# Kernel optimization log

Measured on AMD Instinct MI355X. Metric: run time of the kernel, lower is better.

The kernel has to match this reference:

```python
import jax, jax.numpy as jnp
import numpy as np

B, S, V = 64, 2048, 256

def setup_inputs() -> dict:
    key = jax.random.key(0)
    k1, k2 = jax.random.split(key)
    logits = jax.random.normal(k1, (B, S, V), dtype=jnp.float32)
    prior_knowledge_matrix = jax.random.normal(k2, (V, V), dtype=jnp.float32)
    return {"logits": logits, "prior_knowledge_matrix": prior_knowledge_matrix}

def reference(logits, prior_knowledge_matrix):
    # log-softmax over tag dim
    d = jax.nn.log_softmax(logits, axis=-1)  # [B, S, V]
    # out[b, i] = d[b, i, :] @ M @ d[b, i+1, :]  for i in [0, S-2]
    # fused diagonal-only bilinear form over adjacent positions
    left = jnp.einsum('bsv,vw->bsw', d[:, :-1, :], prior_knowledge_matrix)  # [B, S-1, V]
    out = jnp.einsum('bsw,bsw->bs', left, d[:, 1:, :])  # [B, S-1]
    return out
```

## Files before the change

### kernel.cpp

```cpp
#include <hip/hip_runtime.h>
#include <hip/hip_bf16.h>


#define BQ   32
#define ROWS (BQ + 1)
#define LDA  264

typedef __attribute__((ext_vector_type(8))) short short8;
typedef __attribute__((ext_vector_type(4))) float f32x4;

__device__ __forceinline__ unsigned short f2bf(float f) {
    unsigned int u = __float_as_uint(f);
    unsigned int r = (u + 0x7fffu + ((u >> 16) & 1u)) >> 16;
    return (unsigned short)r;
}
__device__ __forceinline__ float bf2f(unsigned short u) {
    return __uint_as_float(((unsigned int)u) << 16);
}

__global__ void pk_prep(const float* __restrict__ M, unsigned short* __restrict__ mt) {
    int idx = blockIdx.x * 256 + threadIdx.x;
    int n = idx >> 8, k = idx & 255;
    mt[idx] = f2bf(M[k * 256 + n]);
}

__global__ __launch_bounds__(256, 6) void pk_main(const float* __restrict__ logits,
                                                  const unsigned short* __restrict__ mt,
                                                  float* __restrict__ out) {
    __shared__ unsigned short dA[ROWS * LDA];
    __shared__ float partial[BQ][4];

    const int tid  = threadIdx.x;
    const int lane = tid & 63;
    const int wid  = tid >> 6;
    const int b     = blockIdx.x >> 6;
    const int chunk = blockIdx.x & 63;
    const int i0    = chunk * BQ;
    const int nrows = min(ROWS, 2048 - i0);

    const int l15 = lane & 15;
    const int kg  = (lane >> 4) * 8;
    const unsigned short* mw = mt + ((size_t)(wid * 64 + l15)) * 256 + kg;

    {
        const int sub = lane >> 4;
        const float* rowbase = logits + ((size_t)(b * 2048 + i0)) * 256 + l15 * 4;
        const int r0 = wid * 4 + sub;
        const int r1 = 16 + wid * 4 + sub;
        const int r2b = 32 + wid * 4 + sub;
        const bool has2 = (r2b < nrows);

        float4 x0[4], x1[4], x2[4];
        #pragma unroll
        for (int p = 0; p < 4; ++p)
            x0[p] = *reinterpret_cast<const float4*>(rowbase + (size_t)r0 * 256 + p * 64);
        #pragma unroll
        for (int p = 0; p < 4; ++p)
            x1[p] = *reinterpret_cast<const float4*>(rowbase + (size_t)r1 * 256 + p * 64);
        if (has2) {
            #pragma unroll
            for (int p = 0; p < 4; ++p)
                x2[p] = *reinterpret_cast<const float4*>(rowbase + (size_t)r2b * 256 + p * 64);
        }

        {
            float s = 0.f;
            #pragma unroll
            for (int p = 0; p < 4; ++p)
                s += __expf(x0[p].x) + __expf(x0[p].y) + __expf(x0[p].z) + __expf(x0[p].w);
            #pragma unroll
            for (int off = 8; off; off >>= 1) s += __shfl_xor(s, off);
            float lse = __logf(s);
            #pragma unroll
            for (int p = 0; p < 4; ++p) {
                ushort4 pk;
                pk.x = f2bf(x0[p].x - lse); pk.y = f2bf(x0[p].y - lse);
                pk.z = f2bf(x0[p].z - lse); pk.w = f2bf(x0[p].w - lse);
                *reinterpret_cast<ushort4*>(&dA[r0 * LDA + l15 * 4 + p * 64]) = pk;
            }
        }
        {
            float s = 0.f;
            #pragma unroll
            for (int p = 0; p < 4; ++p)
                s += __expf(x1[p].x) + __expf(x1[p].y) + __expf(x1[p].z) + __expf(x1[p].w);
            #pragma unroll
            for (int off = 8; off; off >>= 1) s += __shfl_xor(s, off);
            float lse = __logf(s);
            #pragma unroll
            for (int p = 0; p < 4; ++p) {
                ushort4 pk;
                pk.x = f2bf(x1[p].x - lse); pk.y = f2bf(x1[p].y - lse);
                pk.z = f2bf(x1[p].z - lse); pk.w = f2bf(x1[p].w - lse);
                *reinterpret_cast<ushort4*>(&dA[r1 * LDA + l15 * 4 + p * 64]) = pk;
            }
        }
        if (has2) {
            float s = 0.f;
            #pragma unroll
            for (int p = 0; p < 4; ++p)
                s += __expf(x2[p].x) + __expf(x2[p].y) + __expf(x2[p].z) + __expf(x2[p].w);
            #pragma unroll
            for (int off = 8; off; off >>= 1) s += __shfl_xor(s, off);
            float lse = __logf(s);
            #pragma unroll
            for (int p = 0; p < 4; ++p) {
                ushort4 pk;
                pk.x = f2bf(x2[p].x - lse); pk.y = f2bf(x2[p].y - lse);
                pk.z = f2bf(x2[p].z - lse); pk.w = f2bf(x2[p].w - lse);
                *reinterpret_cast<ushort4*>(&dA[r2b * LDA + l15 * 4 + p * 64]) = pk;
            }
        }
    }

    f32x4 acc[2][4];
    #pragma unroll
    for (int a = 0; a < 2; ++a)
        #pragma unroll
        for (int n = 0; n < 4; ++n) acc[a][n] = (f32x4){0.f, 0.f, 0.f, 0.f};

    short8 bA[4], bB[4];
    #pragma unroll
    for (int n = 0; n < 4; ++n)
        bA[n] = *reinterpret_cast<const short8*>(mw + n * 16 * 256);

    __syncthreads();

    #pragma unroll
    for (int kt = 0; kt < 8; ++kt) {
        short8* cur = (kt & 1) ? bB : bA;
        short8* nxt = (kt & 1) ? bA : bB;
        if (kt < 7) {
            #pragma unroll
            for (int n = 0; n < 4; ++n)
                nxt[n] = *reinterpret_cast<const short8*>(mw + n * 16 * 256 + (kt + 1) * 32);
        }
        short8 aF[2];
        #pragma unroll
        for (int a = 0; a < 2; ++a)
            aF[a] = *reinterpret_cast<const short8*>(&dA[(a * 16 + l15) * LDA + kt * 32 + kg]);
        #pragma unroll
        for (int a = 0; a < 2; ++a)
            #pragma unroll
            for (int n = 0; n < 4; ++n)
                acc[a][n] = __builtin_amdgcn_mfma_f32_16x16x32_bf16(aF[a], cur[n], acc[a][n], 0, 0, 0);
    }

    const int rg = lane >> 4;
    #pragma unroll
    for (int a = 0; a < 2; ++a) {
        #pragma unroll
        for (int r2 = 0; r2 < 4; ++r2) {
            int row = a * 16 + rg * 4 + r2;
            float p = 0.f;
            #pragma unroll
            for (int n = 0; n < 4; ++n) {
                int col = wid * 64 + n * 16 + l15;
                p += acc[a][n][r2] * bf2f(dA[(row + 1) * LDA + col]);
            }
            #pragma unroll
            for (int off = 8; off; off >>= 1) p += __shfl_xor(p, off);
            if (l15 == 0) partial[row][wid] = p;
        }
    }
    __syncthreads();

    if (tid < BQ) {
        float4 pv = *reinterpret_cast<const float4*>(partial[tid]);
        int i = i0 + tid;
        if (i < 2047) out[(size_t)b * 2047 + i] = pv.x + pv.y + pv.z + pv.w;
    }
}

extern "C" void kernel_launch(void* const* d_in, const int* in_sizes, int n_in,
                              void* d_out, int out_size, void* d_ws, size_t ws_size,
                              hipStream_t stream) {
    const float* logits = (const float*)d_in[0];
    const float* M      = (const float*)d_in[1];
    float* out          = (float*)d_out;
    unsigned short* mt  = (unsigned short*)d_ws;

    pk_prep<<<256, 256, 0, stream>>>(M, mt);
    pk_main<<<64 * 64, 256, 0, stream>>>(logits, mt, out);
}
```

Measured before the change: 233.0 us.

## Double row tile to 64 with 8 waves, DPP row reductions, vectorized prep

Each block now handles 64 sequence rows with 512 threads (8 waves), each wave computing 32 output columns over 4 row tiles. The one-row halo reload per block shrinks from 1/32 to 1/64 of the rows, and block count halves. Shuffle-based 16-lane reductions are replaced with DPP row operations, and the matrix transpose/convert prep reads float4 with 64 blocks. The risk is lower occupancy from the larger LDS footprint and bigger blocks, plus fewer blocks for load balancing.

```diff
diff --git a/kernel.cpp b/kernel.cpp
--- a/kernel.cpp
+++ b/kernel.cpp
@@ -2,7 +2,7 @@
 #include <hip/hip_bf16.h>
 
 
-#define BQ   32
+#define BQ   64
 #define ROWS (BQ + 1)
 #define LDA  264
 
@@ -18,49 +18,65 @@
     return __uint_as_float(((unsigned int)u) << 16);
 }
 
+template<int CTRL>
+__device__ __forceinline__ float dpp_xadd(float x) {
+    int y = __builtin_amdgcn_update_dpp(0, __builtin_bit_cast(int, x), CTRL, 0xF, 0xF, true);
+    return x + __builtin_bit_cast(float, y);
+}
+__device__ __forceinline__ float row16_sum(float s) {
+    s = dpp_xadd<0xB1>(s);
+    s = dpp_xadd<0x4E>(s);
+    s = dpp_xadd<0x141>(s);
+    s = dpp_xadd<0x140>(s);
+    return s;
+}
+
 __global__ void pk_prep(const float* __restrict__ M, unsigned short* __restrict__ mt) {
     int idx = blockIdx.x * 256 + threadIdx.x;
-    int n = idx >> 8, k = idx & 255;
-    mt[idx] = f2bf(M[k * 256 + n]);
+    int k  = idx >> 6;
+    int n4 = (idx & 63) * 4;
+    float4 v = *reinterpret_cast<const float4*>(M + (size_t)k * 256 + n4);
+    mt[(n4 + 0) * 256 + k] = f2bf(v.x);
+    mt[(n4 + 1) * 256 + k] = f2bf(v.y);
+    mt[(n4 + 2) * 256 + k] = f2bf(v.z);
+    mt[(n4 + 3) * 256 + k] = f2bf(v.w);
 }
 
-__global__ __launch_bounds__(256, 6) void pk_main(const float* __restrict__ logits,
+__global__ __launch_bounds__(512, 6) void pk_main(const float* __restrict__ logits,
                                                   const unsigned short* __restrict__ mt,
                                                   float* __restrict__ out) {
     __shared__ unsigned short dA[ROWS * LDA];
-    __shared__ float partial[BQ][4];
+    __shared__ float partial[BQ][8];
 
     const int tid  = threadIdx.x;
     const int lane = tid & 63;
     const int wid  = tid >> 6;
-    const int b     = blockIdx.x >> 6;
-    const int chunk = blockIdx.x & 63;
+    const int b     = blockIdx.x >> 5;
+    const int chunk = blockIdx.x & 31;
     const int i0    = chunk * BQ;
     const int nrows = min(ROWS, 2048 - i0);
 
     const int l15 = lane & 15;
-    const int kg  = (lane >> 4) * 8;
-    const unsigned short* mw = mt + ((size_t)(wid * 64 + l15)) * 256 + kg;
+    const int rg  = lane >> 4;
+    const int kg  = rg * 8;
 
     {
-        const int sub = lane >> 4;
         const float* rowbase = logits + ((size_t)(b * 2048 + i0)) * 256 + l15 * 4;
-        const int r0 = wid * 4 + sub;
-        const int r1 = 16 + wid * 4 + sub;
-        const int r2b = 32 + wid * 4 + sub;
-        const bool has2 = (r2b < nrows);
+        const int r0 = wid * 4 + rg;
+        const int r1 = r0 + 32;
+        const bool hasB = (r0 == 0) && (nrows == ROWS);
 
-        float4 x0[4], x1[4], x2[4];
+        float4 x0[4], x1[4], xb[4];
         #pragma unroll
         for (int p = 0; p < 4; ++p)
             x0[p] = *reinterpret_cast<const float4*>(rowbase + (size_t)r0 * 256 + p * 64);
         #pragma unroll
         for (int p = 0; p < 4; ++p)
             x1[p] = *reinterpret_cast<const float4*>(rowbase + (size_t)r1 * 256 + p * 64);
-        if (has2) {
+        if (hasB) {
             #pragma unroll
             for (int p = 0; p < 4; ++p)
-                x2[p] = *reinterpret_cast<const float4*>(rowbase + (size_t)r2b * 256 + p * 64);
+                xb[p] = *reinterpret_cast<const float4*>(rowbase + (size_t)64 * 256 + p * 64);
         }
 
         {
@@ -68,9 +84,7 @@
             #pragma unroll
             for (int p = 0; p < 4; ++p)
                 s += __expf(x0[p].x) + __expf(x0[p].y) + __expf(x0[p].z) + __expf(x0[p].w);
-            #pragma unroll
-            for (int off = 8; off; off >>= 1) s += __shfl_xor(s, off);
-            float lse = __logf(s);
+            float lse = __logf(row16_sum(s));
             #pragma unroll
             for (int p = 0; p < 4; ++p) {
                 ushort4 pk;
@@ -84,9 +98,7 @@
             #pragma unroll
             for (int p = 0; p < 4; ++p)
                 s += __expf(x1[p].x) + __expf(x1[p].y) + __expf(x1[p].z) + __expf(x1[p].w);
-            #pragma unroll
-            for (int off = 8; off; off >>= 1) s += __shfl_xor(s, off);
-            float lse = __logf(s);
+            float lse = __logf(row16_sum(s));
             #pragma unroll
             for (int p = 0; p < 4; ++p) {
                 ushort4 pk;
@@ -95,33 +107,32 @@
                 *reinterpret_cast<ushort4*>(&dA[r1 * LDA + l15 * 4 + p * 64]) = pk;
             }
         }
-        if (has2) {
+        if (hasB) {
             float s = 0.f;
             #pragma unroll
             for (int p = 0; p < 4; ++p)
-                s += __expf(x2[p].x) + __expf(x2[p].y) + __expf(x2[p].z) + __expf(x2[p].w);
-            #pragma unroll
-            for (int off = 8; off; off >>= 1) s += __shfl_xor(s, off);
-            float lse = __logf(s);
+                s += __expf(xb[p].x) + __expf(xb[p].y) + __expf(xb[p].z) + __expf(xb[p].w);
+            float lse = __logf(row16_sum(s));
             #pragma unroll
             for (int p = 0; p < 4; ++p) {
                 ushort4 pk;
-                pk.x = f2bf(x2[p].x - lse); pk.y = f2bf(x2[p].y - lse);
-                pk.z = f2bf(x2[p].z - lse); pk.w = f2bf(x2[p].w - lse);
-                *reinterpret_cast<ushort4*>(&dA[r2b * LDA + l15 * 4 + p * 64]) = pk;
+                pk.x = f2bf(xb[p].x - lse); pk.y = f2bf(xb[p].y - lse);
+                pk.z = f2bf(xb[p].z - lse); pk.w = f2bf(xb[p].w - lse);
+                *reinterpret_cast<ushort4*>(&dA[64 * LDA + l15 * 4 + p * 64]) = pk;
             }
         }
     }
 
-    f32x4 acc[2][4];
+    f32x4 acc[4][2];
     #pragma unroll
-    for (int a = 0; a < 2; ++a)
+    for (int a = 0; a < 4; ++a)
         #pragma unroll
-        for (int n = 0; n < 4; ++n) acc[a][n] = (f32x4){0.f, 0.f, 0.f, 0.f};
+        for (int n = 0; n < 2; ++n) acc[a][n] = (f32x4){0.f, 0.f, 0.f, 0.f};
 
-    short8 bA[4], bB[4];
+    const unsigned short* mw = mt + ((size_t)(wid * 32 + l15)) * 256 + kg;
+    short8 bA[2], bB[2];
     #pragma unroll
-    for (int n = 0; n < 4; ++n)
+    for (int n = 0; n < 2; ++n)
         bA[n] = *reinterpret_cast<const short8*>(mw + n * 16 * 256);
 
     __syncthreads();
@@ -132,43 +143,44 @@
         short8* nxt = (kt & 1) ? bA : bB;
         if (kt < 7) {
             #pragma unroll
-            for (int n = 0; n < 4; ++n)
+            for (int n = 0; n < 2; ++n)
                 nxt[n] = *reinterpret_cast<const short8*>(mw + n * 16 * 256 + (kt + 1) * 32);
         }
-        short8 aF[2];
+        short8 aF[4];
         #pragma unroll
-        for (int a = 0; a < 2; ++a)
+        for (int a = 0; a < 4; ++a)
             aF[a] = *reinterpret_cast<const short8*>(&dA[(a * 16 + l15) * LDA + kt * 32 + kg]);
         #pragma unroll
-        for (int a = 0; a < 2; ++a)
+        for (int a = 0; a < 4; ++a)
             #pragma unroll
-            for (int n = 0; n < 4; ++n)
+            for (int n = 0; n < 2; ++n)
                 acc[a][n] = __builtin_amdgcn_mfma_f32_16x16x32_bf16(aF[a], cur[n], acc[a][n], 0, 0, 0);
     }
 
-    const int rg = lane >> 4;
     #pragma unroll
-    for (int a = 0; a < 2; ++a) {
+    for (int a = 0; a < 4; ++a) {
         #pragma unroll
         for (int r2 = 0; r2 < 4; ++r2) {
             int row = a * 16 + rg * 4 + r2;
             float p = 0.f;
             #pragma unroll
-            for (int n = 0; n < 4; ++n) {
-                int col = wid * 64 + n * 16 + l15;
+            for (int n = 0; n < 2; ++n) {
+                int col = wid * 32 + n * 16 + l15;
                 p += acc[a][n][r2] * bf2f(dA[(row + 1) * LDA + col]);
             }
-            #pragma unroll
-            for (int off = 8; off; off >>= 1) p += __shfl_xor(p, off);
+            p = row16_sum(p);
             if (l15 == 0) partial[row][wid] = p;
         }
     }
     __syncthreads();
 
     if (tid < BQ) {
-        float4 pv = *reinterpret_cast<const float4*>(partial[tid]);
+        float4 p0 = *reinterpret_cast<const float4*>(&partial[tid][0]);
+        float4 p1 = *reinterpret_cast<const float4*>(&partial[tid][4]);
         int i = i0 + tid;
-        if (i < 2047) out[(size_t)b * 2047 + i] = pv.x + pv.y + pv.z + pv.w;
+        if (i < 2047)
+            out[(size_t)b * 2047 + i] = (p0.x + p0.y + p0.z + p0.w)
+                                      + (p1.x + p1.y + p1.z + p1.w);
     }
 }
 
@@ -180,6 +192,6 @@
     float* out          = (float*)d_out;
     unsigned short* mt  = (unsigned short*)d_ws;
 
-    pk_prep<<<256, 256, 0, stream>>>(M, mt);
-    pk_main<<<64 * 64, 256, 0, stream>>>(logits, mt, out);
+    pk_prep<<<64, 256, 0, stream>>>(M, mt);
+    pk_main<<<64 * 32, 512, 0, stream>>>(logits, mt, out);
 }
```

After: 214.3 us. 8.0% less time.
